# Kernel tuning notes

Measured on AMD Instinct MI355X. Metric: run time of the kernel, lower is better.

The kernel has to match this reference:

```python
import jax, jax.numpy as jnp
import numpy as np

WINDOW = 7
NUM_HEADS = 12
DIM = 384


def _relative_position_index(ws):
    coords_h = np.arange(ws)
    coords_w = np.arange(ws)
    coords = np.stack(np.meshgrid(coords_h, coords_w, indexing='ij'))  # [2,ws,ws]
    coords_flatten = coords.transpose(1, 2, 0).reshape(-1, 2)          # [ws*ws,2]
    rel = coords_flatten[:, None, :] - coords_flatten[None, :, :]      # [N,N,2]
    rel[:, :, 0] += ws - 1
    rel[:, :, 1] += ws - 1
    rel[:, :, 0] *= 2 * ws - 1
    return rel.sum(-1).astype(np.int32)                                # [N,N]


def setup_inputs() -> dict:
    key = jax.random.key(0)
    ks = jax.random.split(key, 8)
    B_, N, C, H = 4096, WINDOW * WINDOW, DIM, NUM_HEADS
    x = jax.random.normal(ks[0], (B_, N, C), dtype=jnp.float32)
    mask = jax.random.normal(ks[1], (1, 1, N, N), dtype=jnp.float32)
    qkv_w = jax.random.normal(ks[2], (C, 3 * C), dtype=jnp.float32) * 0.02
    qkv_b = jnp.zeros((3 * C,), dtype=jnp.float32)
    proj_w = jax.random.normal(ks[3], (C, C), dtype=jnp.float32) * 0.02
    proj_b = jnp.zeros((C,), dtype=jnp.float32)
    bias_table = jax.random.normal(ks[4], ((2 * WINDOW - 1) ** 2, H), dtype=jnp.float32) * 0.02
    rel_index = jnp.asarray(_relative_position_index(WINDOW))  # int32 [N,N]
    return {"x": x, "mask": mask, "qkv_w": qkv_w, "qkv_b": qkv_b,
            "proj_w": proj_w, "proj_b": proj_b, "bias_table": bias_table,
            "rel_index": rel_index}


def reference(x, mask, qkv_w, qkv_b, proj_w, proj_b, bias_table, rel_index):
    B_, N, C = x.shape
    H = NUM_HEADS
    hd = C // H
    scale = hd ** (-0.5)
    # qkv projection -> [3, B_, H, N, hd]
    qkv = (x @ qkv_w + qkv_b).reshape(B_, N, 3, H, hd).transpose(2, 0, 3, 1, 4)
    q, k, v = qkv[0], qkv[1], qkv[2]
    attn = jnp.einsum('bhnd,bhmd->bhnm', q, k) * scale  # [B_,H,N,N]
    # gathered relative position bias: [N,N,H] -> [H,N,N]
    bias = bias_table[rel_index].transpose(2, 0, 1)
    attn = attn + bias[None] + mask
    attn = jax.nn.softmax(attn, axis=-1)
    out = jnp.einsum('bhnm,bhmd->bhnd', attn, v)        # [B_,H,N,hd]
    out = out.transpose(0, 2, 1, 3).reshape(B_, N, C)
    return out @ proj_w + proj_b
```

## Files before the change

### kernel.cpp

```cpp
#include <hip/hip_runtime.h>
#include <hip/hip_bf16.h>
#include <stdint.h>

typedef unsigned short u16;
typedef __bf16 bf16x8 __attribute__((ext_vector_type(8)));
typedef float f32x4 __attribute__((ext_vector_type(4)));

#define NWIN 4096
#define NTOK 49
#define CDIM 384
#define NHEAD 12
#define HD 32
#define MROWS (NWIN * NTOK)
#define QKVN (3 * CDIM)
#define SCALE 0.17677669529663689f

__device__ __forceinline__ u16 f2bf(float f) {
  uint32_t u = __float_as_uint(f);
  u += 0x7fff + ((u >> 16) & 1);
  return (u16)(u >> 16);
}

__device__ __forceinline__ void gload_lds16(const void* g, void* l) {
  __builtin_amdgcn_global_load_lds(
      (const __attribute__((address_space(1))) unsigned int*)g,
      (__attribute__((address_space(3))) unsigned int*)l, 16, 0, 0);
}


__global__ __launch_bounds__(256) void cvt_x_kernel(const float* __restrict__ x,
                                                    u16* __restrict__ xb, int n4) {
  int i = blockIdx.x * blockDim.x + threadIdx.x;
  int stride = gridDim.x * blockDim.x;
  for (; i < n4; i += stride) {
    float4 v = ((const float4*)x)[i];
    ushort4 o;
    o.x = f2bf(v.x); o.y = f2bf(v.y); o.z = f2bf(v.z); o.w = f2bf(v.w);
    ((ushort4*)xb)[i] = o;
  }
}

__global__ __launch_bounds__(256) void cvt_wT_kernel(const float* __restrict__ w,
                                                     u16* __restrict__ wT, int K, int N) {
  int i = blockIdx.x * blockDim.x + threadIdx.x;
  if (i >= K * N) return;
  int n = i / K, k = i - n * K;
  wT[i] = f2bf(w[k * N + n]);
}

__global__ __launch_bounds__(256) void build_bias_kernel(const float* __restrict__ bt,
                                                         const int* __restrict__ ri,
                                                         const float* __restrict__ mask,
                                                         float* __restrict__ bias12p) {
  int i = blockIdx.x * blockDim.x + threadIdx.x;
  if (i >= NHEAD * 64 * 64) return;
  int h = i >> 12, r = (i >> 6) & 63, c = i & 63;
  float v = 0.f;
  if (r < NTOK && c < NTOK) v = bt[ri[r * NTOK + c] * NHEAD + h] + mask[r * NTOK + c];
  bias12p[i] = v;
}


template <int MODE>
__global__ __launch_bounds__(256) void gemm128(const u16* __restrict__ A,
                                               const u16* __restrict__ BT,
                                               const float* __restrict__ bias,
                                               float* __restrict__ outF,
                                               u16* __restrict__ q_ws,
                                               u16* __restrict__ k_ws,
                                               u16* __restrict__ vT_ws,
                                               int K, int n_tiles) {
  __shared__ __align__(16) u16 As[2][128 * 64];
  __shared__ __align__(16) u16 Bs[2][128 * 64];
  const int tid = threadIdx.x;
  const int wave = tid >> 6, lane = tid & 63;

  const int nwg = gridDim.x;
  int bid = blockIdx.x;
  bid = (bid & 7) * (nwg >> 3) + (bid >> 3);

  const int mt = bid / n_tiles, ntile = bid - mt * n_tiles;
  const int m0 = mt << 7, n0 = ntile << 7;
  const int fr = lane & 15, fg = lane >> 4;
  const int wr = (wave >> 1) << 6, wc = (wave & 1) << 6;

  f32x4 acc[4][4] = {};

  auto stage = [&](int k0s, int bufi) {
#pragma unroll
    for (int it = 0; it < 4; ++it) {
      const int c = it * 256 + tid;
      const int row = c >> 3, col8 = c & 7;
      const int scol = ((col8 ^ (row & 7)) << 3);
      gload_lds16(A + (size_t)(m0 + row) * K + k0s + scol, &As[bufi][c * 8]);
    }
#pragma unroll
    for (int it = 0; it < 4; ++it) {
      const int c = it * 256 + tid;
      const int row = c >> 3, col8 = c & 7;
      const int scol = ((col8 ^ (row & 7)) << 3);
      gload_lds16(BT + (size_t)(n0 + row) * K + k0s + scol, &Bs[bufi][c * 8]);
    }
  };

  const int nt = K >> 6;
  int cur = 0;

  stage(0, 0);
  __syncthreads();

  for (int t = 0; t < nt; ++t) {
    if (t + 1 < nt) stage((t + 1) << 6, cur ^ 1);

#pragma unroll
    for (int kk = 0; kk < 2; ++kk) {
      bf16x8 av[4], bv[4];
#pragma unroll
      for (int i = 0; i < 4; ++i) {
        const int row = wr + i * 16 + fr;
        const int swz = ((kk << 2) | fg) ^ (fr & 7);
        av[i] = *(const bf16x8*)((const char*)&As[cur][0] + (size_t)row * 128 + (swz << 4));
      }
#pragma unroll
      for (int i = 0; i < 4; ++i) {
        const int row = wc + i * 16 + fr;
        const int swz = ((kk << 2) | fg) ^ (fr & 7);
        bv[i] = *(const bf16x8*)((const char*)&Bs[cur][0] + (size_t)row * 128 + (swz << 4));
      }
      __builtin_amdgcn_s_setprio(1);
#pragma unroll
      for (int i = 0; i < 4; ++i)
#pragma unroll
        for (int j = 0; j < 4; ++j)
          acc[i][j] = __builtin_amdgcn_mfma_f32_16x16x32_bf16(av[i], bv[j], acc[i][j], 0, 0, 0);
      __builtin_amdgcn_s_setprio(0);
    }

    if (t + 1 < nt) __syncthreads();
    cur ^= 1;
  }

#pragma unroll
  for (int j = 0; j < 4; ++j) {
    const int col_g = n0 + wc + j * 16 + fr;
    const float bvadd = bias[col_g];
    if (MODE == 0) {
      const int s = col_g / CDIM;
      const int cr = col_g - s * CDIM;
      const int h = cr >> 5, d = cr & 31;
#pragma unroll
      for (int i = 0; i < 4; ++i) {
#pragma unroll
        for (int r = 0; r < 4; ++r) {
          const int row_g = m0 + wr + i * 16 + fg * 4 + r;
          const int b = row_g / NTOK, n = row_g - b * NTOK;
          const float v = acc[i][j][r] + bvadd;
          const size_t bh = (size_t)b * NHEAD + h;
          if (s == 0)      q_ws[(bh * NTOK + n) * HD + d] = f2bf(v * SCALE);
          else if (s == 1) k_ws[(bh * NTOK + n) * HD + d] = f2bf(v);
          else             vT_ws[(bh * HD + d) * 64 + n] = f2bf(v);
        }
      }
    } else {
#pragma unroll
      for (int i = 0; i < 4; ++i) {
#pragma unroll
        for (int r = 0; r < 4; ++r) {
          const int row_g = m0 + wr + i * 16 + fg * 4 + r;
          outF[(size_t)row_g * CDIM + col_g] = acc[i][j][r] + bvadd;
        }
      }
    }
  }
}


__global__ __launch_bounds__(64) void attn_kernel(const u16* __restrict__ q_ws,
                                                  const u16* __restrict__ k_ws,
                                                  const u16* __restrict__ vT_ws,
                                                  const float* __restrict__ bias12p,
                                                  u16* __restrict__ att_ws) {
  __shared__ __align__(16) float S[64 * 65];
  __shared__ __align__(16) u16 P[64 * 72];
  const int bh = blockIdx.x;
  const int b = bh / NHEAD, h = bh - b * NHEAD;
  const int lane = threadIdx.x;
  const int fr = lane & 15, fg = lane >> 4;
  const u16* qp = q_ws + (size_t)bh * NTOK * HD;
  const u16* kp = k_ws + (size_t)bh * NTOK * HD;
  const u16* vp = vT_ws + (size_t)bh * HD * 64;

  bf16x8 aq[4], bk[4];
#pragma unroll
  for (int i = 0; i < 4; ++i) {
    int m = i * 16 + fr;
    m = m < NTOK ? m : NTOK - 1;
    aq[i] = *(const bf16x8*)&qp[m * HD + fg * 8];
    bk[i] = *(const bf16x8*)&kp[m * HD + fg * 8];
  }
  f32x4 sacc[4][4] = {};
#pragma unroll
  for (int i = 0; i < 4; ++i)
#pragma unroll
    for (int j = 0; j < 4; ++j)
      sacc[i][j] = __builtin_amdgcn_mfma_f32_16x16x32_bf16(aq[i], bk[j], sacc[i][j], 0, 0, 0);

  const float* bp = bias12p + h * 64 * 64;
#pragma unroll
  for (int i = 0; i < 4; ++i)
#pragma unroll
    for (int j = 0; j < 4; ++j)
#pragma unroll
      for (int r = 0; r < 4; ++r) {
        const int row = i * 16 + fg * 4 + r, col = j * 16 + fr;
        S[row * 65 + col] = sacc[i][j][r] + bp[row * 64 + col];
      }
  __syncthreads();

  {
    const int r = lane;
    if (r < NTOK) {
      float mx = -1e30f;
      for (int j = 0; j < NTOK; ++j) mx = fmaxf(mx, S[r * 65 + j]);
      float sum = 0.f;
      for (int j = 0; j < NTOK; ++j) {
        float e = __expf(S[r * 65 + j] - mx);
        sum += e;
        S[r * 65 + j] = e;
      }
      const float inv = 1.f / sum;
      for (int j = 0; j < NTOK; ++j) P[r * 72 + j] = f2bf(S[r * 65 + j] * inv);
      for (int j = NTOK; j < 64; ++j) P[r * 72 + j] = 0;
    } else {
      for (int j = 0; j < 64; ++j) P[r * 72 + j] = 0;
    }
  }
  __syncthreads();

  f32x4 oacc[4][2] = {};
#pragma unroll
  for (int kt = 0; kt < 2; ++kt) {
    bf16x8 ap[4], bv[2];
#pragma unroll
    for (int i = 0; i < 4; ++i)
      ap[i] = *(const bf16x8*)&P[(i * 16 + fr) * 72 + kt * 32 + fg * 8];
#pragma unroll
    for (int n2 = 0; n2 < 2; ++n2)
      bv[n2] = *(const bf16x8*)&vp[(n2 * 16 + fr) * 64 + kt * 32 + fg * 8];
#pragma unroll
    for (int i = 0; i < 4; ++i)
#pragma unroll
      for (int n2 = 0; n2 < 2; ++n2)
        oacc[i][n2] = __builtin_amdgcn_mfma_f32_16x16x32_bf16(ap[i], bv[n2], oacc[i][n2], 0, 0, 0);
  }
  u16* ao = att_ws + ((size_t)b * NTOK) * CDIM + h * HD;
#pragma unroll
  for (int i = 0; i < 4; ++i)
#pragma unroll
    for (int n2 = 0; n2 < 2; ++n2)
#pragma unroll
      for (int r = 0; r < 4; ++r) {
        const int row = i * 16 + fg * 4 + r, col = n2 * 16 + fr;
        if (row < NTOK) ao[(size_t)row * CDIM + col] = f2bf(oacc[i][n2][r]);
      }
}


extern "C" void kernel_launch(void* const* d_in, const int* in_sizes, int n_in,
                              void* d_out, int out_size, void* d_ws, size_t ws_size,
                              hipStream_t stream) {
  (void)in_sizes; (void)n_in; (void)out_size; (void)ws_size;
  const float* x      = (const float*)d_in[0];
  const float* mask   = (const float*)d_in[1];
  const float* qkv_w  = (const float*)d_in[2];
  const float* qkv_b  = (const float*)d_in[3];
  const float* proj_w = (const float*)d_in[4];
  const float* proj_b = (const float*)d_in[5];
  const float* btab   = (const float*)d_in[6];
  const int*   ridx   = (const int*)d_in[7];
  float* out = (float*)d_out;

  char* ws = (char*)d_ws;
  size_t off = 0;
  auto alloc = [&](size_t bytes) {
    char* p = ws + off;
    off = (off + bytes + 255) & ~(size_t)255;
    return p;
  };
  u16* q_ws    = (u16*)alloc((size_t)NWIN * NHEAD * NTOK * HD * 2);
  u16* k_ws    = (u16*)alloc((size_t)NWIN * NHEAD * NTOK * HD * 2);
  u16* vT_ws   = (u16*)alloc((size_t)NWIN * NHEAD * HD * 64 * 2);
  u16* att_ws  = (u16*)alloc((size_t)MROWS * CDIM * 2);
  u16* qkvWT   = (u16*)alloc((size_t)QKVN * CDIM * 2);
  u16* projWT  = (u16*)alloc((size_t)CDIM * CDIM * 2);
  float* bias12p = (float*)alloc((size_t)NHEAD * 64 * 64 * 4);

  u16* x_bf = (u16*)d_out;

  cvt_x_kernel<<<4096, 256, 0, stream>>>(x, x_bf, MROWS * CDIM / 4);
  cvt_wT_kernel<<<(QKVN * CDIM + 255) / 256, 256, 0, stream>>>(qkv_w, qkvWT, CDIM, QKVN);
  cvt_wT_kernel<<<(CDIM * CDIM + 255) / 256, 256, 0, stream>>>(proj_w, projWT, CDIM, CDIM);
  build_bias_kernel<<<(NHEAD * 64 * 64 + 255) / 256, 256, 0, stream>>>(btab, ridx, mask, bias12p);

  gemm128<0><<<(MROWS / 128) * (QKVN / 128), 256, 0, stream>>>(
      x_bf, qkvWT, qkv_b, nullptr, q_ws, k_ws, vT_ws, CDIM, QKVN / 128);

  attn_kernel<<<NWIN * NHEAD, 64, 0, stream>>>(q_ws, k_ws, vT_ws, bias12p, att_ws);

  gemm128<1><<<(MROWS / 128) * (CDIM / 128), 256, 0, stream>>>(
      att_ws, projWT, proj_b, out, nullptr, nullptr, nullptr, CDIM, CDIM / 128);
}
```

Baseline: 1.317 ms.

## Pipeline GEMM with two loads in flight and register-resident softmax in attention

The GEMM now fixes K at compile time, fully unrolls the six K-steps, and prefetches two stages ahead using explicit vmcnt waits and raw barriers in place of __syncthreads. Its epilogue is reordered so each row's four column stores are grouped. The attention kernel loads V fragments up front, and does softmax with the row held in registers, writing P as packed 16-byte LDS stores. S padding also changes from 65 to 66. The aim is to cut load latency stalls and LDS traffic, at the cost of more registers and a hard-coded K.

```diff
diff --git a/kernel.cpp b/kernel.cpp
--- a/kernel.cpp
+++ b/kernel.cpp
@@ -13,6 +13,8 @@
 #define HD 32
 #define MROWS (NWIN * NTOK)
 #define QKVN (3 * CDIM)
+#define GK 384
+#define GNT 6
 #define SCALE 0.17677669529663689f
 
 __device__ __forceinline__ u16 f2bf(float f) {
@@ -69,7 +71,7 @@
                                                u16* __restrict__ q_ws,
                                                u16* __restrict__ k_ws,
                                                u16* __restrict__ vT_ws,
-                                               int K, int n_tiles) {
+                                               int n_tiles) {
   __shared__ __align__(16) u16 As[2][128 * 64];
   __shared__ __align__(16) u16 Bs[2][128 * 64];
   const int tid = threadIdx.x;
@@ -92,26 +94,27 @@
       const int c = it * 256 + tid;
       const int row = c >> 3, col8 = c & 7;
       const int scol = ((col8 ^ (row & 7)) << 3);
-      gload_lds16(A + (size_t)(m0 + row) * K + k0s + scol, &As[bufi][c * 8]);
+      gload_lds16(A + (size_t)(m0 + row) * GK + k0s + scol, &As[bufi][c * 8]);
     }
 #pragma unroll
     for (int it = 0; it < 4; ++it) {
       const int c = it * 256 + tid;
       const int row = c >> 3, col8 = c & 7;
       const int scol = ((col8 ^ (row & 7)) << 3);
-      gload_lds16(BT + (size_t)(n0 + row) * K + k0s + scol, &Bs[bufi][c * 8]);
+      gload_lds16(BT + (size_t)(n0 + row) * GK + k0s + scol, &Bs[bufi][c * 8]);
     }
   };
 
-  const int nt = K >> 6;
-  int cur = 0;
-
   stage(0, 0);
-  __syncthreads();
-
-  for (int t = 0; t < nt; ++t) {
-    if (t + 1 < nt) stage((t + 1) << 6, cur ^ 1);
-
+  stage(64, 1);
+
+#pragma unroll
+  for (int t = 0; t < GNT; ++t) {
+    if (t < GNT - 1) asm volatile("s_waitcnt vmcnt(8)" ::: "memory");
+    else             asm volatile("s_waitcnt vmcnt(0)" ::: "memory");
+    __builtin_amdgcn_s_barrier();
+
+    const int buf = t & 1;
 #pragma unroll
     for (int kk = 0; kk < 2; ++kk) {
       bf16x8 av[4], bv[4];
@@ -119,13 +122,13 @@
       for (int i = 0; i < 4; ++i) {
         const int row = wr + i * 16 + fr;
         const int swz = ((kk << 2) | fg) ^ (fr & 7);
-        av[i] = *(const bf16x8*)((const char*)&As[cur][0] + (size_t)row * 128 + (swz << 4));
+        av[i] = *(const bf16x8*)((const char*)&As[buf][0] + (size_t)row * 128 + (swz << 4));
       }
 #pragma unroll
       for (int i = 0; i < 4; ++i) {
         const int row = wc + i * 16 + fr;
         const int swz = ((kk << 2) | fg) ^ (fr & 7);
-        bv[i] = *(const bf16x8*)((const char*)&Bs[cur][0] + (size_t)row * 128 + (swz << 4));
+        bv[i] = *(const bf16x8*)((const char*)&Bs[buf][0] + (size_t)row * 128 + (swz << 4));
       }
       __builtin_amdgcn_s_setprio(1);
 #pragma unroll
@@ -136,39 +139,49 @@
       __builtin_amdgcn_s_setprio(0);
     }
 
-    if (t + 1 < nt) __syncthreads();
-    cur ^= 1;
-  }
-
-#pragma unroll
-  for (int j = 0; j < 4; ++j) {
-    const int col_g = n0 + wc + j * 16 + fr;
-    const float bvadd = bias[col_g];
-    if (MODE == 0) {
-      const int s = col_g / CDIM;
-      const int cr = col_g - s * CDIM;
-      const int h = cr >> 5, d = cr & 31;
-#pragma unroll
-      for (int i = 0; i < 4; ++i) {
-#pragma unroll
-        for (int r = 0; r < 4; ++r) {
-          const int row_g = m0 + wr + i * 16 + fg * 4 + r;
-          const int b = row_g / NTOK, n = row_g - b * NTOK;
-          const float v = acc[i][j][r] + bvadd;
-          const size_t bh = (size_t)b * NHEAD + h;
-          if (s == 0)      q_ws[(bh * NTOK + n) * HD + d] = f2bf(v * SCALE);
-          else if (s == 1) k_ws[(bh * NTOK + n) * HD + d] = f2bf(v);
-          else             vT_ws[(bh * HD + d) * 64 + n] = f2bf(v);
+    __builtin_amdgcn_s_barrier();
+    if (t + 2 < GNT) stage((t + 2) << 6, buf);
+  }
+
+  const int col0 = n0 + wc + fr;
+  float bvadd[4];
+#pragma unroll
+  for (int j = 0; j < 4; ++j) bvadd[j] = bias[col0 + j * 16];
+
+  if (MODE == 0) {
+    const int s = col0 / CDIM;
+    int hh[4], dd[4];
+#pragma unroll
+    for (int j = 0; j < 4; ++j) {
+      const int cr = col0 + j * 16 - s * CDIM;
+      hh[j] = cr >> 5; dd[j] = cr & 31;
+    }
+#pragma unroll
+    for (int i = 0; i < 4; ++i) {
+#pragma unroll
+      for (int r = 0; r < 4; ++r) {
+        const int row_g = m0 + wr + i * 16 + fg * 4 + r;
+        const int b = row_g / NTOK, n = row_g - b * NTOK;
+        const size_t bhb = (size_t)b * NHEAD;
+#pragma unroll
+        for (int j = 0; j < 4; ++j) {
+          const float v = acc[i][j][r] + bvadd[j];
+          const size_t bh = bhb + hh[j];
+          if (s == 0)      q_ws[(bh * NTOK + n) * HD + dd[j]] = f2bf(v * SCALE);
+          else if (s == 1) k_ws[(bh * NTOK + n) * HD + dd[j]] = f2bf(v);
+          else             vT_ws[(bh * HD + dd[j]) * 64 + n] = f2bf(v);
         }
       }
-    } else {
-#pragma unroll
-      for (int i = 0; i < 4; ++i) {
-#pragma unroll
-        for (int r = 0; r < 4; ++r) {
-          const int row_g = m0 + wr + i * 16 + fg * 4 + r;
-          outF[(size_t)row_g * CDIM + col_g] = acc[i][j][r] + bvadd;
-        }
+    }
+  } else {
+#pragma unroll
+    for (int i = 0; i < 4; ++i) {
+#pragma unroll
+      for (int r = 0; r < 4; ++r) {
+        const int row_g = m0 + wr + i * 16 + fg * 4 + r;
+        float* op = outF + (size_t)row_g * CDIM + col0;
+#pragma unroll
+        for (int j = 0; j < 4; ++j) op[j * 16] = acc[i][j][r] + bvadd[j];
       }
     }
   }
@@ -180,7 +193,7 @@
                                                   const u16* __restrict__ vT_ws,
                                                   const float* __restrict__ bias12p,
                                                   u16* __restrict__ att_ws) {
-  __shared__ __align__(16) float S[64 * 65];
+  __shared__ __align__(16) float S[64 * 66];
   __shared__ __align__(16) u16 P[64 * 72];
   const int bh = blockIdx.x;
   const int b = bh / NHEAD, h = bh - b * NHEAD;
@@ -190,6 +203,13 @@
   const u16* kp = k_ws + (size_t)bh * NTOK * HD;
   const u16* vp = vT_ws + (size_t)bh * HD * 64;
 
+  bf16x8 bv[2][2];
+#pragma unroll
+  for (int kt = 0; kt < 2; ++kt)
+#pragma unroll
+    for (int n2 = 0; n2 < 2; ++n2)
+      bv[kt][n2] = *(const bf16x8*)&vp[(n2 * 16 + fr) * 64 + kt * 32 + fg * 8];
+
   bf16x8 aq[4], bk[4];
 #pragma unroll
   for (int i = 0; i < 4; ++i) {
@@ -213,26 +233,37 @@
 #pragma unroll
       for (int r = 0; r < 4; ++r) {
         const int row = i * 16 + fg * 4 + r, col = j * 16 + fr;
-        S[row * 65 + col] = sacc[i][j][r] + bp[row * 64 + col];
+        S[row * 66 + col] = sacc[i][j][r] + bp[row * 64 + col];
       }
   __syncthreads();
 
   {
     const int r = lane;
-    if (r < NTOK) {
-      float mx = -1e30f;
-      for (int j = 0; j < NTOK; ++j) mx = fmaxf(mx, S[r * 65 + j]);
-      float sum = 0.f;
-      for (int j = 0; j < NTOK; ++j) {
-        float e = __expf(S[r * 65 + j] - mx);
-        sum += e;
-        S[r * 65 + j] = e;
-      }
-      const float inv = 1.f / sum;
-      for (int j = 0; j < NTOK; ++j) P[r * 72 + j] = f2bf(S[r * 65 + j] * inv);
-      for (int j = NTOK; j < 64; ++j) P[r * 72 + j] = 0;
-    } else {
-      for (int j = 0; j < 64; ++j) P[r * 72 + j] = 0;
+    float sv[49];
+#pragma unroll
+    for (int j = 0; j < 49; ++j) sv[j] = S[r * 66 + j];
+    float mx = sv[0];
+#pragma unroll
+    for (int j = 1; j < 49; ++j) mx = fmaxf(mx, sv[j]);
+    float s0 = 0.f, s1 = 0.f;
+#pragma unroll
+    for (int j = 0; j < 48; j += 2) {
+      sv[j]     = __expf(sv[j] - mx);     s0 += sv[j];
+      sv[j + 1] = __expf(sv[j + 1] - mx); s1 += sv[j + 1];
+    }
+    sv[48] = __expf(sv[48] - mx); s0 += sv[48];
+    const float inv = (r < NTOK) ? 1.f / (s0 + s1) : 0.f;
+#pragma unroll
+    for (int c = 0; c < 8; ++c) {
+      uint32_t w[4];
+#pragma unroll
+      for (int u = 0; u < 4; ++u) {
+        const int j0 = c * 8 + u * 2, j1 = j0 + 1;
+        const uint32_t lo = (j0 < 49) ? (uint32_t)f2bf(sv[j0] * inv) : 0u;
+        const uint32_t hi = (j1 < 49) ? (uint32_t)f2bf(sv[j1] * inv) : 0u;
+        w[u] = lo | (hi << 16);
+      }
+      *(uint4*)&P[r * 72 + c * 8] = make_uint4(w[0], w[1], w[2], w[3]);
     }
   }
   __syncthreads();
@@ -240,18 +271,15 @@
   f32x4 oacc[4][2] = {};
 #pragma unroll
   for (int kt = 0; kt < 2; ++kt) {
-    bf16x8 ap[4], bv[2];
+    bf16x8 ap[4];
 #pragma unroll
     for (int i = 0; i < 4; ++i)
       ap[i] = *(const bf16x8*)&P[(i * 16 + fr) * 72 + kt * 32 + fg * 8];
 #pragma unroll
-    for (int n2 = 0; n2 < 2; ++n2)
-      bv[n2] = *(const bf16x8*)&vp[(n2 * 16 + fr) * 64 + kt * 32 + fg * 8];
-#pragma unroll
     for (int i = 0; i < 4; ++i)
 #pragma unroll
       for (int n2 = 0; n2 < 2; ++n2)
-        oacc[i][n2] = __builtin_amdgcn_mfma_f32_16x16x32_bf16(ap[i], bv[n2], oacc[i][n2], 0, 0, 0);
+        oacc[i][n2] = __builtin_amdgcn_mfma_f32_16x16x32_bf16(ap[i], bv[kt][n2], oacc[i][n2], 0, 0, 0);
   }
   u16* ao = att_ws + ((size_t)b * NTOK) * CDIM + h * HD;
 #pragma unroll
@@ -303,10 +331,10 @@
   build_bias_kernel<<<(NHEAD * 64 * 64 + 255) / 256, 256, 0, stream>>>(btab, ridx, mask, bias12p);
 
   gemm128<0><<<(MROWS / 128) * (QKVN / 128), 256, 0, stream>>>(
-      x_bf, qkvWT, qkv_b, nullptr, q_ws, k_ws, vT_ws, CDIM, QKVN / 128);
+      x_bf, qkvWT, qkv_b, nullptr, q_ws, k_ws, vT_ws, QKVN / 128);
 
   attn_kernel<<<NWIN * NHEAD, 64, 0, stream>>>(q_ws, k_ws, vT_ws, bias12p, att_ws);
 
   gemm128<1><<<(MROWS / 128) * (CDIM / 128), 256, 0, stream>>>(
-      att_ws, projWT, proj_b, out, nullptr, nullptr, nullptr, CDIM, CDIM / 128);
-}
+      att_ws, projWT, proj_b, out, nullptr, nullptr, nullptr, CDIM / 128);
+}
```

New measurement: 1.253 ms. -4.8%, faster.
